# Optimization experiments

Measured on AMD Instinct MI355X. Metric: run time of the kernel, lower is better.

## Reference

```python
import jax, jax.numpy as jnp
import numpy as np

TOP_K_PERCENT = 0.25  # top_k_percent_pixels from init_kwargs
B, C, H, W = 8, 19, 512, 1024


def setup_inputs() -> dict:
    key = jax.random.key(0)
    k1, k2 = jax.random.split(key)
    logits = jax.random.normal(k1, (B, C, H, W), dtype=jnp.float32)
    labels = jax.random.randint(k2, (B, H, W), 0, C)  # int labels, in-range
    return {"logits": logits, "labels": labels}


def reference(logits, labels):
    # loss_fn: per-pixel cross-entropy with reduction='none' -> [B, H, W]
    logZ = jax.nn.logsumexp(logits, axis=1)  # [B, H, W], stable softmax normalizer
    gathered = jnp.take_along_axis(logits, labels[:, None, :, :], axis=1)[:, 0]  # [B, H, W]
    loss = logZ - gathered  # per-pixel CE
    # get_topk_percent: flatten non-batch dims, keep top k = pct * num_pixels per row
    flat = loss.reshape(loss.shape[0], -1)  # [B, H*W]
    num_pixels = flat.shape[1]
    k = int(TOP_K_PERCENT * num_pixels)
    top_vals, _ = jax.lax.top_k(flat, k)  # [B, k]
    return top_vals.mean()
```

## Files before the change

kernel.cpp:

```cpp
#include <hip/hip_runtime.h>
#include <cstdint>

#define BB   8
#define CC   19
#define HWP  524288
#define NPIX 4194304
#define KSEL 131072

#define CTRL_OFF 16777216
#define CTRL_WORDS (8*2048 + 8*4096 + 8*256 + 32 + 16)

__global__ void zero_u32(uint32_t* __restrict__ p, int n) {
    int i = blockIdx.x * 256 + threadIdx.x;
    if (i < n) p[i] = 0u;
}

__global__ __launch_bounds__(256) void loss_hist1(
    const float* __restrict__ logits, const int* __restrict__ labels,
    float* __restrict__ loss, uint32_t* __restrict__ hist1)
{
    __shared__ uint32_t lh[2048];
    for (int i = threadIdx.x; i < 2048; i += 256) lh[i] = 0u;
    __syncthreads();

    int b = blockIdx.x >> 9;
    int pix0 = blockIdx.x * 1024 + threadIdx.x * 4;
    int prow = pix0 & (HWP - 1);

    const float4* lg = (const float4*)(logits + (size_t)b * CC * HWP + prow);
    float4 a[CC];
#pragma unroll
    for (int c = 0; c < CC; c++) a[c] = lg[(size_t)c * (HWP / 4)];

    int4 lab = *(const int4*)(labels + pix0);

    float mx0 = a[0].x, mx1 = a[0].y, mx2 = a[0].z, mx3 = a[0].w;
#pragma unroll
    for (int c = 1; c < CC; c++) {
        mx0 = fmaxf(mx0, a[c].x); mx1 = fmaxf(mx1, a[c].y);
        mx2 = fmaxf(mx2, a[c].z); mx3 = fmaxf(mx3, a[c].w);
    }
    float g0 = 0.f, g1 = 0.f, g2 = 0.f, g3 = 0.f;
    float e0 = 0.f, e1 = 0.f, e2 = 0.f, e3 = 0.f;
#pragma unroll
    for (int c = 0; c < CC; c++) {
        e0 += __expf(a[c].x - mx0); e1 += __expf(a[c].y - mx1);
        e2 += __expf(a[c].z - mx2); e3 += __expf(a[c].w - mx3);
        g0 = (lab.x == c) ? a[c].x : g0;
        g1 = (lab.y == c) ? a[c].y : g1;
        g2 = (lab.z == c) ? a[c].z : g2;
        g3 = (lab.w == c) ? a[c].w : g3;
    }
    float l0 = fmaxf(mx0 + __logf(e0) - g0, 0.f);
    float l1 = fmaxf(mx1 + __logf(e1) - g1, 0.f);
    float l2 = fmaxf(mx2 + __logf(e2) - g2, 0.f);
    float l3 = fmaxf(mx3 + __logf(e3) - g3, 0.f);

    float4 o; o.x = l0; o.y = l1; o.z = l2; o.w = l3;
    *(float4*)(loss + pix0) = o;

    atomicAdd(&lh[__float_as_uint(l0) >> 20], 1u);
    atomicAdd(&lh[__float_as_uint(l1) >> 20], 1u);
    atomicAdd(&lh[__float_as_uint(l2) >> 20], 1u);
    atomicAdd(&lh[__float_as_uint(l3) >> 20], 1u);

    __syncthreads();
    for (int i = threadIdx.x; i < 2048; i += 256) {
        uint32_t v = lh[i];
        if (v) atomicAdd(&hist1[b * 2048 + i], v);
    }
}

__global__ void scan_hist(const uint32_t* __restrict__ hist, int nbins,
                          const uint32_t* __restrict__ cntPrev,
                          uint32_t* __restrict__ selOut, uint32_t* __restrict__ cntOut)
{
    int r = blockIdx.x;
    int lane = threadIdx.x & 63;
    int chunk = nbins >> 6;
    const uint32_t* hrow = hist + r * nbins;
    int base = nbins - chunk * (lane + 1);

    uint32_t csum = 0;
    for (int i = 0; i < chunk; i++) csum += hrow[base + i];

    uint32_t inc = csum;
    for (int off = 1; off < 64; off <<= 1) {
        uint32_t t = __shfl_up(inc, off);
        if (lane >= off) inc += t;
    }
    uint32_t pre = inc - csum;

    uint32_t prev = cntPrev ? cntPrev[r] : 0u;
    uint32_t target = (uint32_t)KSEL - prev;

    if (pre < target && pre + csum >= target) {
        uint32_t cum = pre;
        for (int i = chunk - 1; i >= 0; i--) {
            uint32_t h = hrow[base + i];
            if (cum + h >= target) {
                selOut[r] = (uint32_t)(base + i);
                cntOut[r] = prev + cum;
                break;
            }
            cum += h;
        }
    }
}

__device__ __forceinline__ void block_sum_atomic(double sum, double* dst) {
    __shared__ double wsum[4];
    int lane = threadIdx.x & 63, wid = threadIdx.x >> 6;
    for (int off = 32; off > 0; off >>= 1) sum += __shfl_down(sum, off);
    if (lane == 0) wsum[wid] = sum;
    __syncthreads();
    if (threadIdx.x == 0) {
        double t = wsum[0] + wsum[1] + wsum[2] + wsum[3];
        if (t != 0.0) atomicAdd(dst, t);
    }
}

__global__ __launch_bounds__(256) void refine2(
    const float* __restrict__ loss, uint32_t* __restrict__ hist2,
    const uint32_t* __restrict__ sel1, double* __restrict__ sumAbove)
{
    __shared__ uint32_t lh[4096];
    for (int i = threadIdx.x; i < 4096; i += 256) lh[i] = 0u;
    __syncthreads();

    int b = blockIdx.x >> 9;
    uint32_t s1 = sel1[b];
    int pix0 = blockIdx.x * 1024 + threadIdx.x * 4;
    float4 v = *(const float4*)(loss + pix0);

    double sum = 0.0;
    {
        float vv[4] = {v.x, v.y, v.z, v.w};
#pragma unroll
        for (int j = 0; j < 4; j++) {
            uint32_t u = __float_as_uint(vv[j]);
            uint32_t t = u >> 20;
            if (t > s1) sum += (double)vv[j];
            else if (t == s1) atomicAdd(&lh[(u >> 8) & 0xFFFu], 1u);
        }
    }
    __syncthreads();
    block_sum_atomic(sum, &sumAbove[b]);
    for (int i = threadIdx.x; i < 4096; i += 256) {
        uint32_t c = lh[i];
        if (c) atomicAdd(&hist2[b * 4096 + i], c);
    }
}

__global__ __launch_bounds__(256) void refine3(
    const float* __restrict__ loss, uint32_t* __restrict__ hist3,
    const uint32_t* __restrict__ sel1, const uint32_t* __restrict__ sel2,
    double* __restrict__ sumAbove)
{
    __shared__ uint32_t lh[256];
    lh[threadIdx.x] = 0u;
    __syncthreads();

    int b = blockIdx.x >> 9;
    uint32_t s1 = sel1[b], s2 = sel2[b];
    int pix0 = blockIdx.x * 1024 + threadIdx.x * 4;
    float4 v = *(const float4*)(loss + pix0);

    double sum = 0.0;
    {
        float vv[4] = {v.x, v.y, v.z, v.w};
#pragma unroll
        for (int j = 0; j < 4; j++) {
            uint32_t u = __float_as_uint(vv[j]);
            if ((u >> 20) == s1) {
                uint32_t mid = (u >> 8) & 0xFFFu;
                if (mid > s2) sum += (double)vv[j];
                else if (mid == s2) atomicAdd(&lh[u & 0xFFu], 1u);
            }
        }
    }
    __syncthreads();
    block_sum_atomic(sum, &sumAbove[b]);
    {
        uint32_t c = lh[threadIdx.x];
        if (c) atomicAdd(&hist3[b * 256 + threadIdx.x], c);
    }
}

__global__ void finalize(const uint32_t* __restrict__ hist3,
                         const uint32_t* __restrict__ sel1,
                         const uint32_t* __restrict__ sel2,
                         const uint32_t* __restrict__ cnt2,
                         const double* __restrict__ sumAbove,
                         float* __restrict__ out)
{
    __shared__ double rs[8];
    int t = threadIdx.x;
    if (t < 8) {
        int r = t;
        uint32_t rem = (uint32_t)KSEL - cnt2[r];
        double sum = sumAbove[r];
        uint32_t P = (sel1[r] << 20) | (sel2[r] << 8);
        for (int c = 255; c >= 0; c--) {
            uint32_t h = hist3[r * 256 + c];
            if (!h) continue;
            double val = (double)__uint_as_float(P | (uint32_t)c);
            if (h >= rem) { sum += (double)rem * val; rem = 0; break; }
            sum += (double)h * val;
            rem -= h;
        }
        rs[r] = sum;
    }
    __syncthreads();
    if (t == 0) {
        double tot = 0.0;
        for (int i = 0; i < 8; i++) tot += rs[i];
        out[0] = (float)(tot / ((double)BB * (double)KSEL));
    }
}

extern "C" void kernel_launch(void* const* d_in, const int* in_sizes, int n_in,
                              void* d_out, int out_size, void* d_ws, size_t ws_size,
                              hipStream_t stream)
{
    const float* logits = (const float*)d_in[0];
    const int* labels   = (const int*)d_in[1];
    float* out          = (float*)d_out;

    char* ws = (char*)d_ws;
    float* loss      = (float*)ws;
    uint32_t* hist1  = (uint32_t*)(ws + CTRL_OFF);
    uint32_t* hist2  = hist1 + 8 * 2048;
    uint32_t* hist3  = hist2 + 8 * 4096;
    uint32_t* sel1   = hist3 + 8 * 256;
    uint32_t* cnt1   = sel1 + 8;
    uint32_t* sel2   = cnt1 + 8;
    uint32_t* cnt2   = sel2 + 8;
    double* sumAbove = (double*)(cnt2 + 8);

    zero_u32<<<(CTRL_WORDS + 255) / 256, 256, 0, stream>>>(hist1, CTRL_WORDS);
    loss_hist1<<<4096, 256, 0, stream>>>(logits, labels, loss, hist1);
    scan_hist<<<8, 64, 0, stream>>>(hist1, 2048, nullptr, sel1, cnt1);
    refine2<<<4096, 256, 0, stream>>>(loss, hist2, sel1, sumAbove);
    scan_hist<<<8, 64, 0, stream>>>(hist2, 4096, cnt1, sel2, cnt2);
    refine3<<<4096, 256, 0, stream>>>(loss, hist3, sel1, sel2, sumAbove);
    finalize<<<1, 64, 0, stream>>>(hist3, sel1, sel2, cnt2, sumAbove, out);
}
```

Baseline: 580.0 us.

## Fold histogram scans and finalize into last-block tails, use nontemporal loads

Drops the separate scan_hist and finalize launches. The last block of each pass, found with an atomic ticket counter and thread fences, now performs the threshold scan or final reduction using a full 256-thread block scan. The zeroing kernel becomes a hipMemsetAsync, and the logits and labels loads become nontemporal so the single-use stream does not pollute the cache. This cuts launch count and serialization gaps, at the cost of a grid-wide ticket atomic and fence in every block.

```diff
diff --git a/kernel.cpp b/kernel.cpp
--- a/kernel.cpp
+++ b/kernel.cpp
@@ -6,20 +6,94 @@
 #define HWP  524288
 #define NPIX 4194304
 #define KSEL 131072
-
-#define CTRL_OFF 16777216
-#define CTRL_WORDS (8*2048 + 8*4096 + 8*256 + 32 + 16)
-
-__global__ void zero_u32(uint32_t* __restrict__ p, int n) {
-    int i = blockIdx.x * 256 + threadIdx.x;
-    if (i < n) p[i] = 0u;
-}
+#define GRID 4096
+
+typedef float  fx4 __attribute__((ext_vector_type(4)));
+typedef int    ix4 __attribute__((ext_vector_type(4)));
+
+#define H1_OFF   0
+#define H2_OFF   (8*2048)
+#define H3_OFF   (H2_OFF + 8*4096)
+#define SEL1_OFF (H3_OFF + 8*256)
+#define CNT1_OFF (SEL1_OFF + 8)
+#define SEL2_OFF (CNT1_OFF + 8)
+#define CNT2_OFF (SEL2_OFF + 8)
+#define TKT_OFF  (CNT2_OFF + 8)
+#define SUMA_OFF (TKT_OFF + 4)
+#define CTRL_WORDS (SUMA_OFF + 16)
+#define LOSS_BYTES (NPIX * 4)
+
+
+__device__ __forceinline__ uint32_t block_incl_scan_u32(uint32_t v, volatile uint32_t* wt) {
+    int lane = threadIdx.x & 63, wid = threadIdx.x >> 6;
+    uint32_t inc = v;
+#pragma unroll
+    for (int off = 1; off < 64; off <<= 1) {
+        uint32_t t = __shfl_up(inc, off);
+        if (lane >= off) inc += t;
+    }
+    __syncthreads();
+    if (lane == 63) wt[wid] = inc;
+    __syncthreads();
+    for (int w = 0; w < wid; w++) inc += wt[w];
+    return inc;
+}
+
+__device__ __forceinline__ double block_reduce_double(double v, volatile double* dwt) {
+    int lane = threadIdx.x & 63, wid = threadIdx.x >> 6;
+#pragma unroll
+    for (int off = 32; off > 0; off >>= 1) v += __shfl_down(v, off);
+    __syncthreads();
+    if (lane == 0) dwt[wid] = v;
+    __syncthreads();
+    return dwt[0] + dwt[1] + dwt[2] + dwt[3];
+}
+
+template <int NBINS>
+__device__ void scan_rows(const uint32_t* __restrict__ hist,
+                          const uint32_t* __restrict__ cntPrev,
+                          uint32_t* __restrict__ selOut, uint32_t* __restrict__ cntOut,
+                          volatile uint32_t* wt)
+{
+    constexpr int CH = NBINS / 256;
+    for (int r = 0; r < BB; r++) {
+        const uint32_t* hrow = hist + r * NBINS;
+        int base = NBINS - CH * ((int)threadIdx.x + 1);
+        uint32_t hloc[CH];
+        uint32_t csum = 0;
+#pragma unroll
+        for (int i = 0; i < CH; i++) { hloc[i] = hrow[base + i]; csum += hloc[i]; }
+        uint32_t incl = block_incl_scan_u32(csum, wt);
+        uint32_t pre = incl - csum;
+        uint32_t prev = cntPrev ? cntPrev[r] : 0u;
+        uint32_t target = (uint32_t)KSEL - prev;
+        if (pre < target && pre + csum >= target) {
+            uint32_t cum = pre;
+#pragma unroll
+            for (int i = CH - 1; i >= 0; i--) {
+                uint32_t h = hloc[i];
+                if (cum + h >= target) { selOut[r] = (uint32_t)(base + i); cntOut[r] = prev + cum; break; }
+                cum += h;
+            }
+        }
+    }
+}
+
+__device__ __forceinline__ void block_sum_atomic(double sum, double* dst, volatile double* dwt) {
+    double t = block_reduce_double(sum, dwt);
+    if (threadIdx.x == 0 && t != 0.0) atomicAdd(dst, t);
+}
+
 
 __global__ __launch_bounds__(256) void loss_hist1(
     const float* __restrict__ logits, const int* __restrict__ labels,
-    float* __restrict__ loss, uint32_t* __restrict__ hist1)
+    float* __restrict__ loss, uint32_t* __restrict__ ctrl)
 {
     __shared__ uint32_t lh[2048];
+    __shared__ uint32_t wt[4];
+    __shared__ uint32_t isLast;
+    uint32_t* hist1 = ctrl + H1_OFF;
+
     for (int i = threadIdx.x; i < 2048; i += 256) lh[i] = 0u;
     __syncthreads();
 
@@ -27,12 +101,12 @@
     int pix0 = blockIdx.x * 1024 + threadIdx.x * 4;
     int prow = pix0 & (HWP - 1);
 
-    const float4* lg = (const float4*)(logits + (size_t)b * CC * HWP + prow);
-    float4 a[CC];
-#pragma unroll
-    for (int c = 0; c < CC; c++) a[c] = lg[(size_t)c * (HWP / 4)];
-
-    int4 lab = *(const int4*)(labels + pix0);
+    const fx4* lg = (const fx4*)(logits + (size_t)b * CC * HWP + prow);
+    fx4 a[CC];
+#pragma unroll
+    for (int c = 0; c < CC; c++) a[c] = __builtin_nontemporal_load(&lg[(size_t)c * (HWP / 4)]);
+
+    ix4 lab = __builtin_nontemporal_load((const ix4*)(labels + pix0));
 
     float mx0 = a[0].x, mx1 = a[0].y, mx2 = a[0].z, mx3 = a[0].w;
 #pragma unroll
@@ -69,67 +143,33 @@
         uint32_t v = lh[i];
         if (v) atomicAdd(&hist1[b * 2048 + i], v);
     }
-}
-
-__global__ void scan_hist(const uint32_t* __restrict__ hist, int nbins,
-                          const uint32_t* __restrict__ cntPrev,
-                          uint32_t* __restrict__ selOut, uint32_t* __restrict__ cntOut)
-{
-    int r = blockIdx.x;
-    int lane = threadIdx.x & 63;
-    int chunk = nbins >> 6;
-    const uint32_t* hrow = hist + r * nbins;
-    int base = nbins - chunk * (lane + 1);
-
-    uint32_t csum = 0;
-    for (int i = 0; i < chunk; i++) csum += hrow[base + i];
-
-    uint32_t inc = csum;
-    for (int off = 1; off < 64; off <<= 1) {
-        uint32_t t = __shfl_up(inc, off);
-        if (lane >= off) inc += t;
-    }
-    uint32_t pre = inc - csum;
-
-    uint32_t prev = cntPrev ? cntPrev[r] : 0u;
-    uint32_t target = (uint32_t)KSEL - prev;
-
-    if (pre < target && pre + csum >= target) {
-        uint32_t cum = pre;
-        for (int i = chunk - 1; i >= 0; i--) {
-            uint32_t h = hrow[base + i];
-            if (cum + h >= target) {
-                selOut[r] = (uint32_t)(base + i);
-                cntOut[r] = prev + cum;
-                break;
-            }
-            cum += h;
-        }
-    }
-}
-
-__device__ __forceinline__ void block_sum_atomic(double sum, double* dst) {
-    __shared__ double wsum[4];
-    int lane = threadIdx.x & 63, wid = threadIdx.x >> 6;
-    for (int off = 32; off > 0; off >>= 1) sum += __shfl_down(sum, off);
-    if (lane == 0) wsum[wid] = sum;
-    __syncthreads();
-    if (threadIdx.x == 0) {
-        double t = wsum[0] + wsum[1] + wsum[2] + wsum[3];
-        if (t != 0.0) atomicAdd(dst, t);
-    }
-}
+
+    __threadfence();
+    __syncthreads();
+    if (threadIdx.x == 0) isLast = (atomicAdd(ctrl + TKT_OFF + 0, 1u) == GRID - 1);
+    __syncthreads();
+    if (isLast) {
+        __threadfence();
+        scan_rows<2048>(hist1, nullptr, ctrl + SEL1_OFF, ctrl + CNT1_OFF, wt);
+    }
+}
+
 
 __global__ __launch_bounds__(256) void refine2(
-    const float* __restrict__ loss, uint32_t* __restrict__ hist2,
-    const uint32_t* __restrict__ sel1, double* __restrict__ sumAbove)
+    const float* __restrict__ loss, uint32_t* __restrict__ ctrl)
 {
     __shared__ uint32_t lh[4096];
+    __shared__ uint32_t wt[4];
+    __shared__ double dwt[4];
+    __shared__ uint32_t isLast;
+    uint32_t* hist2 = ctrl + H2_OFF;
+    double* sumAbove = (double*)(ctrl + SUMA_OFF);
+
     for (int i = threadIdx.x; i < 4096; i += 256) lh[i] = 0u;
     __syncthreads();
 
     int b = blockIdx.x >> 9;
-    uint32_t s1 = sel1[b];
+    uint32_t s1 = ctrl[SEL1_OFF + b];
     int pix0 = blockIdx.x * 1024 + threadIdx.x * 4;
     float4 v = *(const float4*)(loss + pix0);
 
@@ -145,24 +185,38 @@
         }
     }
     __syncthreads();
-    block_sum_atomic(sum, &sumAbove[b]);
+    block_sum_atomic(sum, &sumAbove[b], dwt);
     for (int i = threadIdx.x; i < 4096; i += 256) {
         uint32_t c = lh[i];
         if (c) atomicAdd(&hist2[b * 4096 + i], c);
     }
-}
+
+    __threadfence();
+    __syncthreads();
+    if (threadIdx.x == 0) isLast = (atomicAdd(ctrl + TKT_OFF + 1, 1u) == GRID - 1);
+    __syncthreads();
+    if (isLast) {
+        __threadfence();
+        scan_rows<4096>(hist2, ctrl + CNT1_OFF, ctrl + SEL2_OFF, ctrl + CNT2_OFF, wt);
+    }
+}
+
 
 __global__ __launch_bounds__(256) void refine3(
-    const float* __restrict__ loss, uint32_t* __restrict__ hist3,
-    const uint32_t* __restrict__ sel1, const uint32_t* __restrict__ sel2,
-    double* __restrict__ sumAbove)
+    const float* __restrict__ loss, uint32_t* __restrict__ ctrl, float* __restrict__ out)
 {
     __shared__ uint32_t lh[256];
+    __shared__ uint32_t wt[4];
+    __shared__ double dwt[4];
+    __shared__ uint32_t isLast;
+    uint32_t* hist3 = ctrl + H3_OFF;
+    double* sumAbove = (double*)(ctrl + SUMA_OFF);
+
     lh[threadIdx.x] = 0u;
     __syncthreads();
 
     int b = blockIdx.x >> 9;
-    uint32_t s1 = sel1[b], s2 = sel2[b];
+    uint32_t s1 = ctrl[SEL1_OFF + b], s2 = ctrl[SEL2_OFF + b];
     int pix0 = blockIdx.x * 1024 + threadIdx.x * 4;
     float4 v = *(const float4*)(loss + pix0);
 
@@ -180,43 +234,33 @@
         }
     }
     __syncthreads();
-    block_sum_atomic(sum, &sumAbove[b]);
+    block_sum_atomic(sum, &sumAbove[b], dwt);
     {
         uint32_t c = lh[threadIdx.x];
         if (c) atomicAdd(&hist3[b * 256 + threadIdx.x], c);
     }
-}
-
-__global__ void finalize(const uint32_t* __restrict__ hist3,
-                         const uint32_t* __restrict__ sel1,
-                         const uint32_t* __restrict__ sel2,
-                         const uint32_t* __restrict__ cnt2,
-                         const double* __restrict__ sumAbove,
-                         float* __restrict__ out)
-{
-    __shared__ double rs[8];
-    int t = threadIdx.x;
-    if (t < 8) {
-        int r = t;
-        uint32_t rem = (uint32_t)KSEL - cnt2[r];
-        double sum = sumAbove[r];
-        uint32_t P = (sel1[r] << 20) | (sel2[r] << 8);
-        for (int c = 255; c >= 0; c--) {
-            uint32_t h = hist3[r * 256 + c];
-            if (!h) continue;
-            double val = (double)__uint_as_float(P | (uint32_t)c);
-            if (h >= rem) { sum += (double)rem * val; rem = 0; break; }
-            sum += (double)h * val;
-            rem -= h;
-        }
-        rs[r] = sum;
-    }
-    __syncthreads();
-    if (t == 0) {
-        double tot = 0.0;
-        for (int i = 0; i < 8; i++) tot += rs[i];
-        out[0] = (float)(tot / ((double)BB * (double)KSEL));
-    }
+
+    __threadfence();
+    __syncthreads();
+    if (threadIdx.x == 0) isLast = (atomicAdd(ctrl + TKT_OFF + 2, 1u) == GRID - 1);
+    __syncthreads();
+    if (!isLast) return;
+    __threadfence();
+
+    double tot = 0.0;
+    for (int r = 0; r < BB; r++) {
+        int b3 = 255 - (int)threadIdx.x;
+        uint32_t h = hist3[r * 256 + b3];
+        uint32_t incl = block_incl_scan_u32(h, wt);
+        uint32_t pre = incl - h;
+        uint32_t rem = (uint32_t)KSEL - ctrl[CNT2_OFF + r];
+        uint32_t take = (rem > pre) ? ((rem - pre < h) ? (rem - pre) : h) : 0u;
+        uint32_t P = (ctrl[SEL1_OFF + r] << 20) | (ctrl[SEL2_OFF + r] << 8) | (uint32_t)b3;
+        double contrib = (double)take * (double)__uint_as_float(P);
+        double s = block_reduce_double(contrib, dwt);
+        if (threadIdx.x == 0) tot += s + sumAbove[r];
+    }
+    if (threadIdx.x == 0) out[0] = (float)(tot / ((double)BB * (double)KSEL));
 }
 
 extern "C" void kernel_launch(void* const* d_in, const int* in_sizes, int n_in,
@@ -228,21 +272,11 @@
     float* out          = (float*)d_out;
 
     char* ws = (char*)d_ws;
-    float* loss      = (float*)ws;
-    uint32_t* hist1  = (uint32_t*)(ws + CTRL_OFF);
-    uint32_t* hist2  = hist1 + 8 * 2048;
-    uint32_t* hist3  = hist2 + 8 * 4096;
-    uint32_t* sel1   = hist3 + 8 * 256;
-    uint32_t* cnt1   = sel1 + 8;
-    uint32_t* sel2   = cnt1 + 8;
-    uint32_t* cnt2   = sel2 + 8;
-    double* sumAbove = (double*)(cnt2 + 8);
-
-    zero_u32<<<(CTRL_WORDS + 255) / 256, 256, 0, stream>>>(hist1, CTRL_WORDS);
-    loss_hist1<<<4096, 256, 0, stream>>>(logits, labels, loss, hist1);
-    scan_hist<<<8, 64, 0, stream>>>(hist1, 2048, nullptr, sel1, cnt1);
-    refine2<<<4096, 256, 0, stream>>>(loss, hist2, sel1, sumAbove);
-    scan_hist<<<8, 64, 0, stream>>>(hist2, 4096, cnt1, sel2, cnt2);
-    refine3<<<4096, 256, 0, stream>>>(loss, hist3, sel1, sel2, sumAbove);
-    finalize<<<1, 64, 0, stream>>>(hist3, sel1, sel2, cnt2, sumAbove, out);
-}
+    float* loss    = (float*)ws;
+    uint32_t* ctrl = (uint32_t*)(ws + LOSS_BYTES);
+
+    (void)hipMemsetAsync(ctrl, 0, CTRL_WORDS * sizeof(uint32_t), stream);
+    loss_hist1<<<GRID, 256, 0, stream>>>(logits, labels, loss, ctrl);
+    refine2<<<GRID, 256, 0, stream>>>(loss, ctrl);
+    refine3<<<GRID, 256, 0, stream>>>(loss, ctrl, out);
+}
```

New measurement: 1.690 ms. 191% more time.
